# Optimization experiments

Measured on AMD Instinct MI355X. Metric: run time of the kernel, lower is better.

Reference implementation:

```python
import jax, jax.numpy as jnp
import numpy as np

F_DIM = 512   # feature_dim
H = 8         # num_heads
D = F_DIM // H  # attention_dim = 64
N = 12288     # total nodes
NP = 6144     # protein nodes (static)
NL = 3072     # ligand nodes (static)
EPS = 1e-5    # LayerNorm eps (torch default)


def setup_inputs() -> dict:
    key = jax.random.key(0)
    ks = jax.random.split(key, 12)
    g = lambda k, shape, s: (jax.random.normal(k, shape, jnp.float32) * s)
    return {
        "h": jax.random.normal(ks[0], (N, F_DIM), jnp.float32),
        # first NP active rows are protein (mask_ligand==0), next NL are ligand, rest inactive
        "mask_ligand": (jnp.arange(N) >= NP).astype(jnp.int32),
        "batch_mask": jnp.arange(N) < (NP + NL),
        "Wp": g(ks[1], (H, F_DIM, D), 0.04),   # per-head protein_linears (no bias)
        "Wl": g(ks[2], (H, F_DIM, D), 0.04),   # per-head ligand_linears (no bias)
        "Up_w": g(ks[3], (H, D, F_DIM), 0.1), "Up_b": g(ks[4], (H, F_DIM), 0.02),
        "Ul_w": g(ks[5], (H, D, F_DIM), 0.1), "Ul_b": g(ks[6], (H, F_DIM), 0.02),
        "ln_w": jnp.ones((D,), jnp.float32), "ln_b": jnp.zeros((D,), jnp.float32),
        "pg_w": g(ks[7], (F_DIM, D), 0.04), "pg_b": jnp.zeros((D,), jnp.float32),
        "lg_w": g(ks[8], (F_DIM, D), 0.04), "lg_b": jnp.zeros((D,), jnp.float32),
        "fb_w": g(ks[9], (D, D), 0.1), "fb_b": jnp.zeros((D,), jnp.float32),
        "fl_w": g(ks[10], (H * F_DIM, F_DIM), 0.015), "fl_b": g(ks[11], (F_DIM,), 0.02),
    }


def _layernorm(x, w, b):
    mu = x.mean(-1, keepdims=True)
    var = ((x - mu) ** 2).mean(-1, keepdims=True)
    return (x - mu) / jnp.sqrt(var + EPS) * w + b


def reference(h, mask_ligand, batch_mask, Wp, Wl, Up_w, Up_b, Ul_w, Ul_b,
              ln_w, ln_b, pg_w, pg_b, lg_w, lg_b, fb_w, fb_b, fl_w, fl_b):
    prot_idx = jnp.nonzero((mask_ligand == 0) & batch_mask, size=NP)[0]
    lig_idx = jnp.nonzero((mask_ligand == 1) & batch_mask, size=NL)[0]
    hp = h[prot_idx]   # [NP, F]
    hl = h[lig_idx]    # [NL, F]

    pf = jnp.einsum('nf,hfd->hnd', hp, Wp)              # per-head protein feats
    lf = jnp.einsum('mf,hfd->hmd', hl, Wl)              # per-head ligand feats
    scores = jnp.einsum('hnd,hmd->hnm', pf, lf) / (D ** 0.5)
    pa = jax.nn.softmax(scores, axis=-1)                # protein attends over ligand
    la = jax.nn.softmax(scores, axis=1)                 # ligand attends over protein
    pc = jnp.einsum('hnm,hmd->hnd', pa, lf)             # protein context
    lc = jnp.einsum('hnm,hnd->hmd', la, pf)             # ligand context

    # gates are head-independent in the original (recomputed identically per head)
    pgate = jax.nn.sigmoid(hp @ pg_w + pg_b)            # [NP, D]
    lgate = jax.nn.sigmoid(hl @ lg_w + lg_b)            # [NL, D]

    pc = jax.nn.sigmoid(_layernorm(pc * pgate, ln_w, ln_b) @ fb_w + fb_b)
    lc = jax.nn.sigmoid(_layernorm(lc * lgate, ln_w, ln_b) @ fb_w + fb_b)

    pout = jnp.einsum('hnd,hdf->hnf', pc, Up_w) + Up_b[:, None, :]
    lout = jnp.einsum('hmd,hdf->hmf', lc, Ul_w) + Ul_b[:, None, :]

    # concat per-head outputs along feature dim, then final projection
    p_final = pout.transpose(1, 0, 2).reshape(NP, H * F_DIM) @ fl_w + fl_b
    l_final = lout.transpose(1, 0, 2).reshape(NL, H * F_DIM) @ fl_w + fl_b

    h_updated = h.at[prot_idx].set(p_final + hp)
    h_updated = h_updated.at[lig_idx].set(l_final + hl)
    return h_updated
```

## Files before the change

### kernel.cpp

```cpp
#include <hip/hip_runtime.h>
#include <hip/hip_bf16.h>
#include <cstdint>
#include <cstddef>

#define F_DIM 512
#define NHEAD 8
#define DD 64
#define NPROT 6144
#define NLIG 3072
#define NACT 9216
#define NTOT 12288

typedef unsigned short u16;
typedef __attribute__((ext_vector_type(8))) short bf8;
typedef __attribute__((ext_vector_type(4))) float f4;
typedef __attribute__((ext_vector_type(16))) float f16f;
typedef __attribute__((ext_vector_type(2))) unsigned int u32x2;

__device__ __forceinline__ u16 f2bf(float f){
  union { float f; uint32_t u; } v; v.f = f;
  uint32_t r = v.u + 0x7fffu + ((v.u >> 16) & 1u);
  return (u16)(r >> 16);
}
__device__ __forceinline__ float bf2f(u16 s){
  union { uint32_t u; float f; } v; v.u = ((uint32_t)s) << 16; return v.f;
}

__device__ __forceinline__ f4 mfma16(bf8 a, bf8 b, f4 c){
  return __builtin_amdgcn_mfma_f32_16x16x32_bf16(a, b, c, 0, 0, 0);
}

__device__ __forceinline__ float exp2_fast(float x){
  float r;
  asm("v_exp_f32 %0, %1\n\ts_nop 1" : "=v"(r) : "v"(x));
  return r;
}
__device__ __forceinline__ uint32_t cvtpk(float a, float b){
  uint32_t r;
  asm("v_cvt_pk_bf16_f32 %0, %1, %2" : "=v"(r) : "v"(a), "v"(b));
  return r;
}

__global__ void k_cvt(const float* __restrict__ in, u16* __restrict__ out, int n4){
  int i = blockIdx.x * blockDim.x + threadIdx.x;
  if (i >= n4) return;
  float4 v = ((const float4*)in)[i];
  union { u16 u[4]; uint64_t q; } pk;
  pk.u[0]=f2bf(v.x); pk.u[1]=f2bf(v.y); pk.u[2]=f2bf(v.z); pk.u[3]=f2bf(v.w);
  ((uint64_t*)out)[i] = pk.q;
}

__global__ __launch_bounds__(256) void k_cvtT64(const float* __restrict__ in,
                                                u16* __restrict__ out, int R, int C){
  __shared__ u16 T[64][65];
  int64_t base = (int64_t)blockIdx.z * R * C;
  int cb = blockIdx.x*64, rb = blockIdx.y*64;
  #pragma unroll
  for (int i=0;i<16;i++){
    int idx = i*256 + threadIdx.x;
    int r = idx>>6, c = idx&63;
    T[r][c] = f2bf(in[base + (int64_t)(rb+r)*C + cb + c]);
  }
  __syncthreads();
  #pragma unroll
  for (int i=0;i<16;i++){
    int idx = i*256 + threadIdx.x;
    int c = idx>>6, r = idx&63;
    out[base + (int64_t)(cb+c)*R + rb + r] = T[r][c];
  }
}

__global__ __launch_bounds__(256) void k_proj(const u16* __restrict__ hb,
    const u16* __restrict__ WpT, const u16* __restrict__ WlT,
    u16* __restrict__ pf, u16* __restrict__ pfT,
    u16* __restrict__ lfb, u16* __restrict__ lfT){
  int pass = blockIdx.z;
  if (pass == 1 && blockIdx.x >= NLIG/64) return;
  int M = pass ? NLIG : NPROT;
  const u16* A  = hb + (pass ? (size_t)NPROT*F_DIM : 0);
  const u16* BT = pass ? WlT : WpT;
  u16* P  = pass ? lfb : pf;
  u16* PT = pass ? lfT : pfT;
  int h = blockIdx.y;
  int w = threadIdx.x >> 6, lane = threadIdx.x & 63;
  int lr = lane & 15, lkg = lane >> 4, lk = lkg * 8;
  int rb = blockIdx.x * 64;
  const u16* Ap = A + (size_t)(rb + w*16 + lr) * F_DIM + lk;
  const u16* Bp = BT + (size_t)h * DD * F_DIM + (size_t)lr * F_DIM + lk;
  f4 acc[4] = {};
  for (int k = 0; k < F_DIM; k += 32){
    bf8 a = *(const bf8*)(Ap + k);
    #pragma unroll
    for (int cf = 0; cf < 4; cf++){
      bf8 b = *(const bf8*)(Bp + (size_t)cf*16*F_DIM + k);
      acc[cf] = mfma16(a, b, acc[cf]);
    }
  }
  __shared__ u16 T[64*72];
  #pragma unroll
  for (int cf = 0; cf < 4; cf++){
    int d = cf*16 + lr;
    #pragma unroll
    for (int r = 0; r < 4; r++){
      u16 v = f2bf(acc[cf][r]);
      int rl = w*16 + lkg*4 + r;
      P[(size_t)h*M*DD + (size_t)(rb+rl)*DD + d] = v;
      T[rl*72 + d] = v;
    }
  }
  __syncthreads();
  int d = threadIdx.x >> 2, j = threadIdx.x & 3;
  union { u16 u[16]; bf8 v[2]; } pk;
  #pragma unroll
  for (int uu = 0; uu < 16; uu++) pk.u[uu] = T[(j*16+uu)*72 + d];
  bf8* dst = (bf8*)(PT + ((size_t)h*DD + d)*M + rb + j*16);
  dst[0] = pk.v[0]; dst[1] = pk.v[1];
}

__global__ __launch_bounds__(256) void k_gate(const u16* __restrict__ hb,
    const u16* __restrict__ pgT, const u16* __restrict__ lgT,
    const float* __restrict__ pgb, const float* __restrict__ lgb,
    float* __restrict__ pgate, float* __restrict__ lgate){
  int pass = blockIdx.z;
  if (pass == 1 && blockIdx.x >= NLIG/64) return;
  const u16* A  = hb + (pass ? (size_t)NPROT*F_DIM : 0);
  const u16* BT = pass ? lgT : pgT;
  const float* gb = pass ? lgb : pgb;
  float* outp = pass ? lgate : pgate;
  int w = threadIdx.x>>6, lane = threadIdx.x&63, lr = lane&15, lkg = lane>>4, lk = lkg*8;
  int rb = blockIdx.x*64;
  const u16* Ap = A + (size_t)(rb + w*16 + lr)*F_DIM + lk;
  const u16* Bp = BT + (size_t)lr*F_DIM + lk;
  f4 acc[4] = {};
  for (int k=0;k<F_DIM;k+=32){
    bf8 a = *(const bf8*)(Ap+k);
    #pragma unroll
    for (int cf=0;cf<4;cf++){
      bf8 b = *(const bf8*)(Bp + (size_t)cf*16*F_DIM + k);
      acc[cf]=mfma16(a,b,acc[cf]);
    }
  }
  int r0 = rb + w*16 + lkg*4;
  #pragma unroll
  for (int cf=0;cf<4;cf++){
    int d = cf*16+lr; float bb = gb[d];
    #pragma unroll
    for (int r=0;r<4;r++){
      float z = acc[cf][r] + bb;
      outp[(size_t)(r0+r)*DD + d] = 1.f/(1.f + __expf(-z));
    }
  }
}

__global__ __launch_bounds__(256) void k_mw(const u16* __restrict__ UpWb, const u16* __restrict__ UlWb,
    const u16* __restrict__ flT, u16* __restrict__ MpT, u16* __restrict__ MlT){
  const u16* A = blockIdx.z ? UlWb : UpWb;
  u16* O = blockIdx.z ? MlT : MpT;
  int h = blockIdx.y;
  int fobase = blockIdx.x * 64;
  int w = threadIdx.x>>6, lane = threadIdx.x&63, lr = lane&15, lkg = lane>>4, lk = lkg*8;
  const u16* Ap = A + (size_t)h*DD*F_DIM + (size_t)(w*16+lr)*F_DIM + lk;
  const u16* Bp = flT + (size_t)(fobase+lr)*(NHEAD*F_DIM) + (size_t)h*F_DIM + lk;
  f4 acc[4] = {};
  for (int k=0;k<F_DIM;k+=32){
    bf8 a = *(const bf8*)(Ap+k);
    #pragma unroll
    for (int cf=0;cf<4;cf++){
      bf8 b = *(const bf8*)(Bp + (size_t)cf*16*(NHEAD*F_DIM) + k);
      acc[cf]=mfma16(a,b,acc[cf]);
    }
  }
  int d0 = w*16 + lkg*4;
  #pragma unroll
  for (int cf=0;cf<4;cf++){
    int fo = fobase + cf*16 + lr;
    #pragma unroll
    for (int r=0;r<4;r++)
      O[(size_t)fo*F_DIM + h*DD + d0 + r] = f2bf(acc[cf][r]);
  }
}

__global__ void k_cinit(const float* __restrict__ flb, float* __restrict__ cp, float* __restrict__ cl){
  int i = blockIdx.x*blockDim.x + threadIdx.x;
  if (i < F_DIM){ cp[i] = flb[i]; cl[i] = flb[i]; }
}
__global__ void k_cacc(const float* __restrict__ flw, const float* __restrict__ Upb,
    const float* __restrict__ Ulb, float* __restrict__ cp, float* __restrict__ cl){
  const float* bias = blockIdx.z ? Ulb : Upb;
  float* o = blockIdx.z ? cl : cp;
  int fo = blockIdx.y*256 + threadIdx.x;
  int r0 = blockIdx.x*128;
  float acc = 0.f;
  #pragma unroll 4
  for (int r = r0; r < r0+128; r++) acc += bias[r] * flw[(size_t)r*F_DIM + fo];
  atomicAdd(o + fo, acc);
}

__global__ __launch_bounds__(256, 2) void k_attn(
    const u16* __restrict__ pf, const u16* __restrict__ lfb,
    const u16* __restrict__ pfT, const u16* __restrict__ lfT,
    float* __restrict__ pnum, float* __restrict__ pden,
    float* __restrict__ lnum, float* __restrict__ lden){
  int bid = blockIdx.x;
  int pass = (bid < 384);
  int NQ, NK, qt, h;
  const u16 *Q, *Kt, *Vt; float *num, *den;
  if (pass){
    qt = bid >> 3; h = bid & 7;
    NQ = NLIG; NK = NPROT; Q = lfb; Kt = pf; Vt = pfT; num = lnum; den = lden;
  } else {
    int l = bid - 384; qt = l >> 3; h = l & 7;
    NQ = NPROT; NK = NLIG; Q = pf; Kt = lfb; Vt = lfT; num = pnum; den = pden;
  }
  int wv = threadIdx.x>>6, lane = threadIdx.x&63;
  int ql = lane&31, hi = lane>>5;
  int qsub = wv & 1, kvh = wv >> 1;
  int qg = qt*64 + qsub*32 + ql;
  int nt = NK >> 6;
  int kv0 = kvh * (NK >> 1);
  const u16* Qh = Q + (size_t)h*NQ*DD;
  const u16* Kh = Kt + (size_t)h*NK*DD;
  const u16* Vh = Vt + (size_t)h*DD*NK;
  const float SC = 0.125f * 1.44269504088896f;

  bf8 qf[4];
  #pragma unroll
  for (int kk=0;kk<4;kk++){
    union { bf8 v; u16 s[8]; uint32_t u[4]; } qr, qo;
    qr.v = *(const bf8*)(Qh + (size_t)qg*DD + kk*16 + hi*8);
    #pragma unroll
    for (int j=0;j<4;j++)
      qo.u[j] = cvtpk(bf2f(qr.s[2*j])*SC, bf2f(qr.s[2*j+1])*SC);
    qf[kk] = qo.v;
  }

  f16f o0 = {}, o1 = {};
  float dsum = 0.f;
  const u16* Kp  = Kh + (size_t)(kv0 + ql)*DD + hi*8;
  const u16* Vp0 = Vh + (size_t)ql*NK + kv0 + hi*8;
  const u16* Vp1 = Vh + (size_t)(32+ql)*NK + kv0 + hi*8;

  for (int t=0; t<nt; t++){
    f16f s = {};
    #pragma unroll
    for (int kk=0;kk<4;kk++){
      bf8 kf = *(const bf8*)(Kp + kk*16);
      s = __builtin_amdgcn_mfma_f32_32x32x16_bf16(kf, qf[kk], s, 0, 0, 0);
    }
    float e[16];
    #pragma unroll
    for (int r=0;r<16;r++){ e[r] = exp2_fast(s[r]); dsum += e[r]; }
    union { uint32_t u[4]; bf8 v; } B0, B1;
    {
      u32x2 p;
      p = __builtin_amdgcn_permlane32_swap(cvtpk(e[0],e[1]),   cvtpk(e[4],e[5]),   false, false);
      B0.u[0]=p[0]; B0.u[2]=p[1];
      p = __builtin_amdgcn_permlane32_swap(cvtpk(e[2],e[3]),   cvtpk(e[6],e[7]),   false, false);
      B0.u[1]=p[0]; B0.u[3]=p[1];
      p = __builtin_amdgcn_permlane32_swap(cvtpk(e[8],e[9]),   cvtpk(e[12],e[13]), false, false);
      B1.u[0]=p[0]; B1.u[2]=p[1];
      p = __builtin_amdgcn_permlane32_swap(cvtpk(e[10],e[11]), cvtpk(e[14],e[15]), false, false);
      B1.u[1]=p[0]; B1.u[3]=p[1];
    }
    bf8 v00 = *(const bf8*)(Vp0);
    bf8 v01 = *(const bf8*)(Vp0 + 16);
    bf8 v10 = *(const bf8*)(Vp1);
    bf8 v11 = *(const bf8*)(Vp1 + 16);
    o0 = __builtin_amdgcn_mfma_f32_32x32x16_bf16(v00, B0.v, o0, 0, 0, 0);
    o0 = __builtin_amdgcn_mfma_f32_32x32x16_bf16(v01, B1.v, o0, 0, 0, 0);
    o1 = __builtin_amdgcn_mfma_f32_32x32x16_bf16(v10, B0.v, o1, 0, 0, 0);
    o1 = __builtin_amdgcn_mfma_f32_32x32x16_bf16(v11, B1.v, o1, 0, 0, 0);
    Kp += 32*DD; Vp0 += 32; Vp1 += 32;
  }

  __shared__ float Cmb[2][2][64][16];
  __shared__ float Dls[2][64];
  if (wv >= 2){
    union { f16f v; f4 q[4]; } a0, a1;
    a0.v = o0; a1.v = o1;
    f4* c0 = (f4*)&Cmb[qsub][0][lane][0];
    f4* c1 = (f4*)&Cmb[qsub][1][lane][0];
    #pragma unroll
    for (int r4=0;r4<4;r4++){ c0[r4] = a0.q[r4]; c1[r4] = a1.q[r4]; }
    Dls[qsub][lane] = dsum;
  }
  __syncthreads();
  if (wv < 2){
    f4* c0 = (f4*)&Cmb[qsub][0][lane][0];
    f4* c1 = (f4*)&Cmb[qsub][1][lane][0];
    union { f16f v; f4 q[4]; } b0, b1;
    b0.v = o0; b1.v = o1;
    #pragma unroll
    for (int r4=0;r4<4;r4++){
      f4 t0 = c0[r4], t1 = c1[r4];
      b0.q[r4] += t0; b1.q[r4] += t1;
    }
    dsum += Dls[qsub][lane];
    dsum += __shfl_xor(dsum, 32, 64);
    float* np = num + ((size_t)h*NQ + qg)*DD;
    #pragma unroll
    for (int r4=0;r4<4;r4++){
      *(f4*)(np + r4*8 + 4*hi)      = b0.q[r4];
      *(f4*)(np + 32 + r4*8 + 4*hi) = b1.q[r4];
    }
    if (hi == 0) den[(size_t)h*NQ + qg] = dsum;
  }
}

__global__ __launch_bounds__(256) void k_post(
    const float* __restrict__ pnum, const float* __restrict__ pden,
    const float* __restrict__ lnum, const float* __restrict__ lden,
    const float* __restrict__ pgate, const float* __restrict__ lgate,
    const float* __restrict__ lnw, const float* __restrict__ lnb,
    const u16* __restrict__ fbT, const float* __restrict__ fbb,
    u16* __restrict__ pc2, u16* __restrict__ lc2){
  int t = blockIdx.x;
  int pass = (t >= NPROT/64);
  int h = blockIdx.y;
  int NQ = pass ? NLIG : NPROT;
  const float* num = pass ? lnum : pnum;
  const float* den = pass ? lden : pden;
  const float* gate = pass ? lgate : pgate;
  u16* oc = pass ? lc2 : pc2;
  int qbase = (pass ? t - NPROT/64 : t) * 64;

  __shared__ u16 Pl[64*72];
  int w = threadIdx.x>>6, lane = threadIdx.x&63;
  int lr = lane&15, lkg = lane>>4, lk = lkg*8;
  u16* Pw = Pl + (w*16)*72;
  int orow0 = qbase + w*16 + lkg*4;

  float rd[4];
  #pragma unroll
  for (int r=0;r<4;r++) rd[r] = 1.f / den[(size_t)h*NQ + orow0 + r];

  float v[4][4];
  #pragma unroll
  for (int cf=0;cf<4;cf++){
    int d = cf*16+lr;
    #pragma unroll
    for (int r=0;r<4;r++)
      v[cf][r] = num[((size_t)h*NQ + orow0 + r)*DD + d] * rd[r]
               * gate[(size_t)(orow0+r)*DD + d];
  }
  float m1[4], m2[4];
  #pragma unroll
  for (int r=0;r<4;r++){
    float s1 = v[0][r]+v[1][r]+v[2][r]+v[3][r];
    float s2 = v[0][r]*v[0][r]+v[1][r]*v[1][r]+v[2][r]*v[2][r]+v[3][r]*v[3][r];
    s1 += __shfl_xor(s1,1,64); s2 += __shfl_xor(s2,1,64);
    s1 += __shfl_xor(s1,2,64); s2 += __shfl_xor(s2,2,64);
    s1 += __shfl_xor(s1,4,64); s2 += __shfl_xor(s2,4,64);
    s1 += __shfl_xor(s1,8,64); s2 += __shfl_xor(s2,8,64);
    float mu = s1 * (1.f/64.f);
    float var = s2 * (1.f/64.f) - mu*mu;
    if (var < 0.f) var = 0.f;
    m1[r] = mu; m2[r] = rsqrtf(var + 1e-5f);
  }
  #pragma unroll
  for (int cf=0;cf<4;cf++){
    int d = cf*16+lr;
    float lw = lnw[d], lb = lnb[d];
    #pragma unroll
    for (int r=0;r<4;r++){
      float n = (v[cf][r]-m1[r])*m2[r]*lw + lb;
      Pw[(lkg*4+r)*72 + d] = f2bf(n);
    }
  }
  f4 z4[4] = {};
  #pragma unroll
  for (int kc=0;kc<2;kc++){
    bf8 pa = *(const bf8*)(Pw + lr*72 + kc*32 + lk);
    #pragma unroll
    for (int cf=0;cf<4;cf++){
      bf8 b = *(const bf8*)(fbT + (size_t)(cf*16+lr)*DD + kc*32 + lk);
      z4[cf] = mfma16(pa, b, z4[cf]);
    }
  }
  #pragma unroll
  for (int cf=0;cf<4;cf++){
    int d = cf*16+lr;
    float bb = fbb[d];
    #pragma unroll
    for (int r=0;r<4;r++){
      float sg = 1.f/(1.f + __expf(-(z4[cf][r] + bb)));
      oc[(size_t)(orow0+r)*F_DIM + h*DD + d] = f2bf(sg);
    }
  }
}

__global__ __launch_bounds__(256) void k_final(const float* __restrict__ hsrc,
    const u16* __restrict__ pc2, const u16* __restrict__ lc2,
    const u16* __restrict__ MpT, const u16* __restrict__ MlT,
    const float* __restrict__ cp, const float* __restrict__ cl,
    float* __restrict__ out){
  int R = blockIdx.x*64;
  int cbase = blockIdx.y*64;
  int tid = threadIdx.x;
  if (R >= NACT){
    int r = tid>>2, s0 = tid&3;
    const float4* hp4 = (const float4*)(hsrc + (size_t)(R+r)*F_DIM + cbase);
    float4* op4 = (float4*)(out + (size_t)(R+r)*F_DIM + cbase);
    #pragma unroll
    for (int s=0;s<4;s++) op4[s0 + s*4] = hp4[s0 + s*4];
    return;
  }
  bool isP = (R < NPROT);
  const u16* A = isP ? (pc2 + (size_t)R*F_DIM) : (lc2 + (size_t)(R-NPROT)*F_DIM);
  const u16* B = isP ? MpT : MlT;
  const float* cv = isP ? cp : cl;
  int w = tid>>6, lane = tid&63, lr = lane&15, lkg = lane>>4, lk = lkg*8;
  const u16* Ap = A + (size_t)(w*16+lr)*F_DIM + lk;
  const u16* Bp = B + (size_t)(cbase+lr)*F_DIM + lk;
  f4 acc[4] = {};
  for (int k=0;k<F_DIM;k+=32){
    bf8 a = *(const bf8*)(Ap+k);
    #pragma unroll
    for (int cf=0;cf<4;cf++){
      bf8 b = *(const bf8*)(Bp + (size_t)cf*16*F_DIM + k);
      acc[cf]=mfma16(a,b,acc[cf]);
    }
  }
  int row0 = R + w*16 + lkg*4;
  #pragma unroll
  for (int cf=0;cf<4;cf++){
    int c = cbase + cf*16 + lr;
    float cc = cv[c];
    #pragma unroll
    for (int r=0;r<4;r++)
      out[(size_t)(row0+r)*F_DIM + c] = acc[cf][r] + cc + hsrc[(size_t)(row0+r)*F_DIM + c];
  }
}

extern "C" void kernel_launch(void* const* d_in, const int* in_sizes, int n_in,
                              void* d_out, int out_size, void* d_ws, size_t ws_size,
                              hipStream_t stream){
  (void)in_sizes; (void)n_in; (void)out_size; (void)ws_size;
  const float* h    = (const float*)d_in[0];
  const float* Wp   = (const float*)d_in[3];
  const float* Wl   = (const float*)d_in[4];
  const float* Upw  = (const float*)d_in[5];
  const float* Upb  = (const float*)d_in[6];
  const float* Ulw  = (const float*)d_in[7];
  const float* Ulb  = (const float*)d_in[8];
  const float* lnw  = (const float*)d_in[9];
  const float* lnb  = (const float*)d_in[10];
  const float* pgw  = (const float*)d_in[11];
  const float* pgb  = (const float*)d_in[12];
  const float* lgw  = (const float*)d_in[13];
  const float* lgb  = (const float*)d_in[14];
  const float* fbw  = (const float*)d_in[15];
  const float* fbb  = (const float*)d_in[16];
  const float* flw  = (const float*)d_in[17];
  const float* flb  = (const float*)d_in[18];
  float* out = (float*)d_out;

  char* wsp = (char*)d_ws;
  size_t off = 0;
  auto alloc = [&](size_t b)->char* {
    char* p = wsp + off; off = (off + b + 255) & ~(size_t)255; return p;
  };
  u16* hb    = (u16*)alloc((size_t)NACT*F_DIM*2);
  u16* WpT   = (u16*)alloc((size_t)NHEAD*DD*F_DIM*2);
  u16* WlT   = (u16*)alloc((size_t)NHEAD*DD*F_DIM*2);
  u16* pgT   = (u16*)alloc((size_t)DD*F_DIM*2);
  u16* lgT   = (u16*)alloc((size_t)DD*F_DIM*2);
  u16* fbT   = (u16*)alloc((size_t)DD*DD*2);
  u16* UpWb  = (u16*)alloc((size_t)NHEAD*DD*F_DIM*2);
  u16* UlWb  = (u16*)alloc((size_t)NHEAD*DD*F_DIM*2);
  u16* flT   = (u16*)alloc((size_t)F_DIM*NHEAD*F_DIM*2);
  u16* pf    = (u16*)alloc((size_t)NHEAD*NPROT*DD*2);
  u16* pfT   = (u16*)alloc((size_t)NHEAD*DD*NPROT*2);
  u16* lfb   = (u16*)alloc((size_t)NHEAD*NLIG*DD*2);
  u16* lfT   = (u16*)alloc((size_t)NHEAD*DD*NLIG*2);
  float* pgate = (float*)alloc((size_t)NPROT*DD*4);
  float* lgate = (float*)alloc((size_t)NLIG*DD*4);
  u16* pc2   = (u16*)alloc((size_t)NPROT*F_DIM*2);
  u16* lc2   = (u16*)alloc((size_t)NLIG*F_DIM*2);
  u16* MpT   = (u16*)alloc((size_t)F_DIM*F_DIM*2);
  u16* MlT   = (u16*)alloc((size_t)F_DIM*F_DIM*2);
  float* cp  = (float*)alloc(F_DIM*4);
  float* cl  = (float*)alloc(F_DIM*4);
  size_t n_pnum = (size_t)NHEAD*NPROT*DD, n_lnum = (size_t)NHEAD*NLIG*DD;
  size_t n_pden = (size_t)NHEAD*NPROT,     n_lden = (size_t)NHEAD*NLIG;
  float* pnum = (float*)alloc(n_pnum*4);
  float* lnum = (float*)alloc(n_lnum*4);
  float* pden = (float*)alloc(n_pden*4);
  float* lden = (float*)alloc(n_lden*4);

  k_cvt<<<dim3((NACT*F_DIM/4 + 255)/256), 256, 0, stream>>>(h, hb, NACT*F_DIM/4);
  k_cvt<<<dim3((NHEAD*DD*F_DIM/4 + 255)/256), 256, 0, stream>>>(Upw, UpWb, NHEAD*DD*F_DIM/4);
  k_cvt<<<dim3((NHEAD*DD*F_DIM/4 + 255)/256), 256, 0, stream>>>(Ulw, UlWb, NHEAD*DD*F_DIM/4);
  k_cvtT64<<<dim3(1, 8, NHEAD), 256, 0, stream>>>(Wp, WpT, F_DIM, DD);
  k_cvtT64<<<dim3(1, 8, NHEAD), 256, 0, stream>>>(Wl, WlT, F_DIM, DD);
  k_cvtT64<<<dim3(1, 8, 1), 256, 0, stream>>>(pgw, pgT, F_DIM, DD);
  k_cvtT64<<<dim3(1, 8, 1), 256, 0, stream>>>(lgw, lgT, F_DIM, DD);
  k_cvtT64<<<dim3(1, 1, 1), 256, 0, stream>>>(fbw, fbT, DD, DD);
  k_cvtT64<<<dim3(8, 64, 1), 256, 0, stream>>>(flw, flT, NHEAD*F_DIM, F_DIM);

  k_proj<<<dim3(NPROT/64, NHEAD, 2), 256, 0, stream>>>(hb, WpT, WlT, pf, pfT, lfb, lfT);
  k_gate<<<dim3(NPROT/64, 1, 2), 256, 0, stream>>>(hb, pgT, lgT, pgb, lgb, pgate, lgate);
  k_mw<<<dim3(F_DIM/64, NHEAD, 2), 256, 0, stream>>>(UpWb, UlWb, flT, MpT, MlT);
  k_cinit<<<dim3(2), 256, 0, stream>>>(flb, cp, cl);
  k_cacc<<<dim3(32, 2, 2), 256, 0, stream>>>(flw, Upb, Ulb, cp, cl);

  k_attn<<<dim3(1152), 256, 0, stream>>>(pf, lfb, pfT, lfT, pnum, pden, lnum, lden);
  k_post<<<dim3(NPROT/64 + NLIG/64, NHEAD), 256, 0, stream>>>(
      pnum, pden, lnum, lden, pgate, lgate, lnw, lnb, fbT, fbb, pc2, lc2);
  k_final<<<dim3(NTOT/64, F_DIM/64), 256, 0, stream>>>(h, pc2, lc2, MpT, MlT, cp, cl, out);
}
```

Baseline: 542.4 us.

## Split attention KV range across four waves and fuse gate GEMM into projection

The attention kernel now gives each block 32 queries, with all four waves splitting the key range into quarters. This doubles the grid to 2304 blocks and raises the occupancy hint to 6 blocks per CU. Partial outputs are merged by a two-step tree reduction through shared memory, which adds extra barriers. Separately, the gate GEMM is folded into the projection kernel as a ninth head slice, removing one kernel launch.

```diff
diff --git a/kernel.cpp b/kernel.cpp
--- a/kernel.cpp
+++ b/kernel.cpp
@@ -73,29 +73,48 @@
 __global__ __launch_bounds__(256) void k_proj(const u16* __restrict__ hb,
     const u16* __restrict__ WpT, const u16* __restrict__ WlT,
     u16* __restrict__ pf, u16* __restrict__ pfT,
-    u16* __restrict__ lfb, u16* __restrict__ lfT){
+    u16* __restrict__ lfb, u16* __restrict__ lfT,
+    const u16* __restrict__ pgT, const u16* __restrict__ lgT,
+    const float* __restrict__ pgb, const float* __restrict__ lgb,
+    float* __restrict__ pgate, float* __restrict__ lgate){
   int pass = blockIdx.z;
   if (pass == 1 && blockIdx.x >= NLIG/64) return;
   int M = pass ? NLIG : NPROT;
   const u16* A  = hb + (pass ? (size_t)NPROT*F_DIM : 0);
-  const u16* BT = pass ? WlT : WpT;
-  u16* P  = pass ? lfb : pf;
-  u16* PT = pass ? lfT : pfT;
   int h = blockIdx.y;
   int w = threadIdx.x >> 6, lane = threadIdx.x & 63;
   int lr = lane & 15, lkg = lane >> 4, lk = lkg * 8;
   int rb = blockIdx.x * 64;
   const u16* Ap = A + (size_t)(rb + w*16 + lr) * F_DIM + lk;
-  const u16* Bp = BT + (size_t)h * DD * F_DIM + (size_t)lr * F_DIM + lk;
+  const u16* BT;
+  if (h == 8) BT = (pass ? lgT : pgT) + (size_t)lr * F_DIM + lk;
+  else        BT = (pass ? WlT : WpT) + (size_t)h * DD * F_DIM + (size_t)lr * F_DIM + lk;
   f4 acc[4] = {};
   for (int k = 0; k < F_DIM; k += 32){
     bf8 a = *(const bf8*)(Ap + k);
     #pragma unroll
     for (int cf = 0; cf < 4; cf++){
-      bf8 b = *(const bf8*)(Bp + (size_t)cf*16*F_DIM + k);
+      bf8 b = *(const bf8*)(BT + (size_t)cf*16*F_DIM + k);
       acc[cf] = mfma16(a, b, acc[cf]);
     }
   }
+  if (h == 8){
+    const float* gb = pass ? lgb : pgb;
+    float* outp = pass ? lgate : pgate;
+    int r0 = rb + w*16 + lkg*4;
+    #pragma unroll
+    for (int cf=0;cf<4;cf++){
+      int d = cf*16+lr; float bb = gb[d];
+      #pragma unroll
+      for (int r=0;r<4;r++){
+        float z = acc[cf][r] + bb;
+        outp[(size_t)(r0+r)*DD + d] = 1.f/(1.f + __expf(-z));
+      }
+    }
+    return;
+  }
+  u16* P  = pass ? lfb : pf;
+  u16* PT = pass ? lfT : pfT;
   __shared__ u16 T[64*72];
   #pragma unroll
   for (int cf = 0; cf < 4; cf++){
@@ -115,41 +134,6 @@
   for (int uu = 0; uu < 16; uu++) pk.u[uu] = T[(j*16+uu)*72 + d];
   bf8* dst = (bf8*)(PT + ((size_t)h*DD + d)*M + rb + j*16);
   dst[0] = pk.v[0]; dst[1] = pk.v[1];
-}
-
-__global__ __launch_bounds__(256) void k_gate(const u16* __restrict__ hb,
-    const u16* __restrict__ pgT, const u16* __restrict__ lgT,
-    const float* __restrict__ pgb, const float* __restrict__ lgb,
-    float* __restrict__ pgate, float* __restrict__ lgate){
-  int pass = blockIdx.z;
-  if (pass == 1 && blockIdx.x >= NLIG/64) return;
-  const u16* A  = hb + (pass ? (size_t)NPROT*F_DIM : 0);
-  const u16* BT = pass ? lgT : pgT;
-  const float* gb = pass ? lgb : pgb;
-  float* outp = pass ? lgate : pgate;
-  int w = threadIdx.x>>6, lane = threadIdx.x&63, lr = lane&15, lkg = lane>>4, lk = lkg*8;
-  int rb = blockIdx.x*64;
-  const u16* Ap = A + (size_t)(rb + w*16 + lr)*F_DIM + lk;
-  const u16* Bp = BT + (size_t)lr*F_DIM + lk;
-  f4 acc[4] = {};
-  for (int k=0;k<F_DIM;k+=32){
-    bf8 a = *(const bf8*)(Ap+k);
-    #pragma unroll
-    for (int cf=0;cf<4;cf++){
-      bf8 b = *(const bf8*)(Bp + (size_t)cf*16*F_DIM + k);
-      acc[cf]=mfma16(a,b,acc[cf]);
-    }
-  }
-  int r0 = rb + w*16 + lkg*4;
-  #pragma unroll
-  for (int cf=0;cf<4;cf++){
-    int d = cf*16+lr; float bb = gb[d];
-    #pragma unroll
-    for (int r=0;r<4;r++){
-      float z = acc[cf][r] + bb;
-      outp[(size_t)(r0+r)*DD + d] = 1.f/(1.f + __expf(-z));
-    }
-  }
 }
 
 __global__ __launch_bounds__(256) void k_mw(const u16* __restrict__ UpWb, const u16* __restrict__ UlWb,
@@ -196,28 +180,27 @@
   atomicAdd(o + fo, acc);
 }
 
-__global__ __launch_bounds__(256, 2) void k_attn(
+__global__ __launch_bounds__(256, 6) void k_attn(
     const u16* __restrict__ pf, const u16* __restrict__ lfb,
     const u16* __restrict__ pfT, const u16* __restrict__ lfT,
     float* __restrict__ pnum, float* __restrict__ pden,
     float* __restrict__ lnum, float* __restrict__ lden){
   int bid = blockIdx.x;
-  int pass = (bid < 384);
+  int pass = (bid < 768);
   int NQ, NK, qt, h;
   const u16 *Q, *Kt, *Vt; float *num, *den;
   if (pass){
     qt = bid >> 3; h = bid & 7;
     NQ = NLIG; NK = NPROT; Q = lfb; Kt = pf; Vt = pfT; num = lnum; den = lden;
   } else {
-    int l = bid - 384; qt = l >> 3; h = l & 7;
+    int l = bid - 768; qt = l >> 3; h = l & 7;
     NQ = NPROT; NK = NLIG; Q = pf; Kt = lfb; Vt = lfT; num = pnum; den = pden;
   }
   int wv = threadIdx.x>>6, lane = threadIdx.x&63;
   int ql = lane&31, hi = lane>>5;
-  int qsub = wv & 1, kvh = wv >> 1;
-  int qg = qt*64 + qsub*32 + ql;
-  int nt = NK >> 6;
-  int kv0 = kvh * (NK >> 1);
+  int qg = qt*32 + ql;
+  int nt = NK >> 7;
+  int kv0 = wv * (NK >> 2);
   const u16* Qh = Q + (size_t)h*NQ*DD;
   const u16* Kh = Kt + (size_t)h*NK*DD;
   const u16* Vh = Vt + (size_t)h*DD*NK;
@@ -273,35 +256,44 @@
     Kp += 32*DD; Vp0 += 32; Vp1 += 32;
   }
 
-  __shared__ float Cmb[2][2][64][16];
+  __shared__ float Cmb[2][64][36];
   __shared__ float Dls[2][64];
-  if (wv >= 2){
-    union { f16f v; f4 q[4]; } a0, a1;
-    a0.v = o0; a1.v = o1;
-    f4* c0 = (f4*)&Cmb[qsub][0][lane][0];
-    f4* c1 = (f4*)&Cmb[qsub][1][lane][0];
-    #pragma unroll
-    for (int r4=0;r4<4;r4++){ c0[r4] = a0.q[r4]; c1[r4] = a1.q[r4]; }
-    Dls[qsub][lane] = dsum;
+  union { f16f v; f4 q[4]; } a0, a1;
+  a0.v = o0; a1.v = o1;
+  if (wv & 1){
+    int slot = wv >> 1;
+    f4* c = (f4*)&Cmb[slot][lane][0];
+    #pragma unroll
+    for (int r4=0;r4<4;r4++){ c[r4] = a0.q[r4]; c[r4+4] = a1.q[r4]; }
+    Dls[slot][lane] = dsum;
   }
   __syncthreads();
-  if (wv < 2){
-    f4* c0 = (f4*)&Cmb[qsub][0][lane][0];
-    f4* c1 = (f4*)&Cmb[qsub][1][lane][0];
-    union { f16f v; f4 q[4]; } b0, b1;
-    b0.v = o0; b1.v = o1;
-    #pragma unroll
-    for (int r4=0;r4<4;r4++){
-      f4 t0 = c0[r4], t1 = c1[r4];
-      b0.q[r4] += t0; b1.q[r4] += t1;
-    }
-    dsum += Dls[qsub][lane];
+  if (!(wv & 1)){
+    int slot = wv >> 1;
+    f4* c = (f4*)&Cmb[slot][lane][0];
+    #pragma unroll
+    for (int r4=0;r4<4;r4++){ a0.q[r4] += c[r4]; a1.q[r4] += c[r4+4]; }
+    dsum += Dls[slot][lane];
+  }
+  __syncthreads();
+  if (wv == 2){
+    f4* c = (f4*)&Cmb[1][lane][0];
+    #pragma unroll
+    for (int r4=0;r4<4;r4++){ c[r4] = a0.q[r4]; c[r4+4] = a1.q[r4]; }
+    Dls[1][lane] = dsum;
+  }
+  __syncthreads();
+  if (wv == 0){
+    f4* c = (f4*)&Cmb[1][lane][0];
+    #pragma unroll
+    for (int r4=0;r4<4;r4++){ a0.q[r4] += c[r4]; a1.q[r4] += c[r4+4]; }
+    dsum += Dls[1][lane];
     dsum += __shfl_xor(dsum, 32, 64);
     float* np = num + ((size_t)h*NQ + qg)*DD;
     #pragma unroll
     for (int r4=0;r4<4;r4++){
-      *(f4*)(np + r4*8 + 4*hi)      = b0.q[r4];
-      *(f4*)(np + 32 + r4*8 + 4*hi) = b1.q[r4];
+      *(f4*)(np + r4*8 + 4*hi)      = a0.q[r4];
+      *(f4*)(np + 32 + r4*8 + 4*hi) = a1.q[r4];
     }
     if (hi == 0) den[(size_t)h*NQ + qg] = dsum;
   }
@@ -498,13 +490,13 @@
   k_cvtT64<<<dim3(1, 1, 1), 256, 0, stream>>>(fbw, fbT, DD, DD);
   k_cvtT64<<<dim3(8, 64, 1), 256, 0, stream>>>(flw, flT, NHEAD*F_DIM, F_DIM);
 
-  k_proj<<<dim3(NPROT/64, NHEAD, 2), 256, 0, stream>>>(hb, WpT, WlT, pf, pfT, lfb, lfT);
-  k_gate<<<dim3(NPROT/64, 1, 2), 256, 0, stream>>>(hb, pgT, lgT, pgb, lgb, pgate, lgate);
+  k_proj<<<dim3(NPROT/64, NHEAD+1, 2), 256, 0, stream>>>(hb, WpT, WlT, pf, pfT, lfb, lfT,
+                                                         pgT, lgT, pgb, lgb, pgate, lgate);
   k_mw<<<dim3(F_DIM/64, NHEAD, 2), 256, 0, stream>>>(UpWb, UlWb, flT, MpT, MlT);
   k_cinit<<<dim3(2), 256, 0, stream>>>(flb, cp, cl);
   k_cacc<<<dim3(32, 2, 2), 256, 0, stream>>>(flw, Upb, Ulb, cp, cl);
 
-  k_attn<<<dim3(1152), 256, 0, stream>>>(pf, lfb, pfT, lfT, pnum, pden, lnum, lden);
+  k_attn<<<dim3(2304), 256, 0, stream>>>(pf, lfb, pfT, lfT, pnum, pden, lnum, lden);
   k_post<<<dim3(NPROT/64 + NLIG/64, NHEAD), 256, 0, stream>>>(
       pnum, pden, lnum, lden, pgate, lgate, lnw, lnb, fbT, fbb, pc2, lc2);
   k_final<<<dim3(NTOT/64, F_DIM/64), 256, 0, stream>>>(h, pc2, lc2, MpT, MlT, cp, cl, out);
```

Result: slower. 611.4 us (+12.7%).
